# Performance work log

Hardware: AMD Instinct MI355X
Metric: run time of the kernel (lower is better)

Reference implementation:

```python
import jax, jax.numpy as jnp
import numpy as np

# hyperparameters (init_kwargs)
T = 0.1
MARGIN = 0.0
NEG_IOU = 0.5
K = 2              # pos_topk
WEIGHT = 1.0
EXPONENT = 2.0
NEG_SAMPLES = 512  # neg_samples_num
START_DNS_EPOCH = 1

# static problem sizes
B, SPB, TPS = 16, 2, 4          # videos, sentences/video, targets/sentence
N, C = 64, 256                  # clips, channels
S = B * SPB                     # total sentences = 32
M = S * TPS                     # total moments = 128


def setup_inputs() -> dict:
    key = jax.random.key(0)
    k1, k2, k3, k4 = jax.random.split(key, 4)
    return {
        "video_feats": jax.random.normal(k1, (S, C, N, N), jnp.float32),
        "sents_feats": jax.random.normal(k2, (S, C), jnp.float32),
        "num_sentences": jnp.full((B,), SPB, jnp.int32),
        "num_targets": jnp.full((S,), TPS, jnp.int32),
        "iou2d": jax.random.uniform(k3, (S, N, N), jnp.float32),
        "iou2ds": jax.random.uniform(k4, (M, N, N), jnp.float32),
        "mask2d": jnp.triu(jnp.ones((N, N), bool)),  # 2D-TAN valid-proposal mask
        "epoch": 2,
    }


def _normalize(x):
    return x / jnp.maximum(jnp.linalg.norm(x, axis=-1, keepdims=True), 1e-12)


def _loss_core(video_feats, sents_feats, iou2d, iou2ds,
               num_sentences, num_targets, mask2d, epoch):
    S_, C_, N_, _ = video_feats.shape
    B_ = num_sentences.shape[0]
    M_ = iou2ds.shape[0]
    P = N_ * (N_ + 1) // 2  # number of True in upper-triangular mask2d

    # masked_select(mask2d) -> gather flat proposal positions (static size P)
    flat_idx = jnp.nonzero(mask2d.reshape(-1), size=P)[0]
    vf = video_feats.reshape(S_, C_, N_ * N_)[:, :, flat_idx]        # (S,C,P)
    vf = _normalize(vf.transpose(0, 2, 1))                            # (S,P,C)
    _ = _normalize(sents_feats)                                       # normalized but unused downstream
    iou2d_f = iou2d.reshape(S_, -1)[:, flat_idx]                      # (S,P)
    iou2ds_f = iou2ds.reshape(M_, -1)[:, flat_idx]                    # (M,P)

    scatter_m2s = jnp.repeat(jnp.arange(S_), num_targets, total_repeat_length=M_)
    scatter_s2b = jnp.repeat(jnp.arange(B_), num_sentences, total_repeat_length=S_)
    scatter_b2s = jnp.concatenate([jnp.zeros((1,), jnp.int32),
                                   jnp.cumsum(num_sentences)[:-1].astype(jnp.int32)])

    # all (ref, pos) pairs within each sentence's num_targets*K topk slots (uniform -> static)
    nK = (M_ // S_) * K
    base = (jnp.arange(S_) * nK)[:, None, None]
    i = jnp.arange(nK)
    zero = jnp.zeros((nK,), jnp.int32)
    ref_idx = (base + i[None, :, None] + zero[None, None, :]).reshape(-1)   # (E,)
    pos_idx = (base + zero[None, :, None] + i[None, None, :]).reshape(-1)   # (E,)
    scatter_e2s = jnp.repeat(jnp.arange(S_), nK * nK)                        # (E,)

    # top-K proposals per moment by IoU
    topk_idx = jax.lax.top_k(iou2ds_f, K)[1]                                 # (M,K)
    allm = vf[scatter_m2s]                                                   # (M,P,C)
    topk_vf = jnp.take_along_axis(allm, topk_idx[:, :, None], axis=1)        # (M,K,C)
    pos_vf = topk_vf.reshape(M_ * K, C_)

    intra_pos = jnp.sum(pos_vf[ref_idx] * pos_vf[pos_idx], axis=-1)          # (E,)
    bank = vf[scatter_b2s].reshape(B_ * P, C_)                               # one sentence per video
    intra_all = pos_vf @ bank.T                                              # (M*K, B*P)

    # positive mask: own-video block, refined by iou2d > neg_iou
    own = scatter_s2b[:, None] == jnp.arange(B_)[None, :]                    # (S,B)
    s2v_pos = iou2d_f > NEG_IOU                                              # (S,P)
    pos_mask = jnp.where(own[:, :, None], s2v_pos[:, None, :], False).reshape(S_, B_ * P)

    if epoch >= START_DNS_EPOCH:
        # DNS: similarity-weighted negative sampling without replacement (Gumbel top-k)
        sim = (jnp.einsum('mkc,pc->mkp', topk_vf, bank).mean(axis=1) + 1.0) * 0.5   # (M,B*P)
        fused = jax.ops.segment_sum(sim, scatter_m2s, num_segments=S_)
        fused = fused / num_targets[:, None].astype(sim.dtype)                      # per-sentence mean
        fused = jnp.where(pos_mask, 0.0, fused ** EXPONENT)                          # (S,B*P)
        logw = jnp.where(fused > 0, jnp.log(jnp.maximum(fused, 1e-30)), -jnp.inf)
        u = jax.random.uniform(jax.random.key(42), fused.shape, minval=1e-7, maxval=1.0 - 1e-7)
        gumbel = -jnp.log(-jnp.log(u))
        samp_idx = jax.lax.top_k(logw + gumbel, NEG_SAMPLES)[1]                      # (S,NEG_SAMPLES)
        neg_mask = jnp.zeros((S_, B_ * P), jnp.float32).at[
            jnp.arange(S_)[:, None], samp_idx].set(1.0)
    else:
        neg_mask = (~pos_mask).astype(jnp.float32)

    # LogCrossEntropy (InfoNCE with explicit negative mask)
    all_e = intra_all[ref_idx]            # (E, B*P)
    neg_e = neg_mask[scatter_e2s]         # (E, B*P)
    pos_logit = (intra_pos - MARGIN) / T
    neg_sum = jnp.sum(jnp.exp(all_e / T) * neg_e, axis=-1)
    loss = jnp.mean(-(pos_logit - jnp.log(jnp.exp(pos_logit) + neg_sum)))
    return loss


def reference(video_feats, sents_feats, num_sentences, num_targets,
              iou2d, iou2ds, mask2d, epoch):
    loss = _loss_core(video_feats, sents_feats, iou2d, iou2ds,
                      num_sentences, num_targets, mask2d, epoch)
    return (loss * WEIGHT, loss)
```

## Files before the change

kernel.cpp:

```cpp
#include <hip/hip_runtime.h>
#include <math.h>
#include <stdint.h>

#define S_    32
#define BV_   16
#define M_    128
#define C_    256
#define NN    4096
#define P_    2080
#define BP    33280
#define NSAMP 512
#define CHUNK 130

__device__ __forceinline__ uint32_t rotl32(uint32_t x, int n){ return (x<<n) | (x>>(32-n)); }

__device__ __forceinline__ void threefry2x32(uint32_t k0, uint32_t k1, uint32_t &x0, uint32_t &x1){
  uint32_t ks2 = k0 ^ k1 ^ 0x1BD11BDAu;
  x0 += k0; x1 += k1;
  #define TF_R(r) { x0 += x1; x1 = rotl32(x1, r); x1 ^= x0; }
  TF_R(13) TF_R(15) TF_R(26) TF_R(6)
  x0 += k1;  x1 += ks2 + 1u;
  TF_R(17) TF_R(29) TF_R(16) TF_R(24)
  x0 += ks2; x1 += k0 + 2u;
  TF_R(13) TF_R(15) TF_R(26) TF_R(6)
  x0 += k0;  x1 += k1 + 3u;
  TF_R(17) TF_R(29) TF_R(16) TF_R(24)
  x0 += k1;  x1 += ks2 + 4u;
  TF_R(13) TF_R(15) TF_R(26) TF_R(6)
  x0 += ks2; x1 += k0 + 5u;
  #undef TF_R
}

__device__ __forceinline__ void p_to_ij(int p, int &i, int &j){
  i = (int)((129.0f - sqrtf((float)(16641 - 8*p))) * 0.5f);
  while(64*(i+1) - ((i+1)*i)/2 <= p) ++i;
  while(64*i - (i*(i-1))/2 > p) --i;
  j = i + (p - (64*i - (i*(i-1))/2));
}

__global__ __launch_bounds__(256) void k_prep(const float* __restrict__ iou2ds,
                                              const float* __restrict__ vfeat,
                                              float* __restrict__ pos_vf,
                                              float* __restrict__ qsumT){
  const int s = blockIdx.x;
  const int t = threadIdx.x;
  __shared__ float sv1[256], sv2[256];
  __shared__ int   si1[256], si2[256];
  __shared__ int   fpk_s[8];
  __shared__ float wsum[4];
  __shared__ float s_inv;

  for(int q=0; q<4; ++q){
    const float* row = iou2ds + (size_t)(s*4 + q)*NN;
    float v1=-1e30f, v2=-1e30f; int i1=0x7FFFFFFF, i2=0x7FFFFFFF;
    for(int f=t; f<NN; f+=256){
      int ti = f>>6, tj = f&63;
      if(tj < ti) continue;
      float v = row[f];
      if(v > v1 || (v == v1 && f < i1)){ v2=v1; i2=i1; v1=v; i1=f; }
      else if(v > v2 || (v == v2 && f < i2)){ v2=v; i2=f; }
    }
    sv1[t]=v1; sv2[t]=v2; si1[t]=i1; si2[t]=i2;
    for(int stp=128; stp>0; stp>>=1){
      __syncthreads();
      if(t < stp){
        float a1=sv1[t], a2=sv2[t]; int x1=si1[t], x2=si2[t];
        float b1=sv1[t+stp], b2=sv2[t+stp]; int y1=si1[t+stp], y2=si2[t+stp];
        float m1v, m2v; int m1i, m2i;
        bool aTop = (a1 > b1) || (a1 == b1 && x1 < y1);
        if(aTop){
          m1v=a1; m1i=x1;
          if((a2 > b1) || (a2 == b1 && x2 < y1)){ m2v=a2; m2i=x2; } else { m2v=b1; m2i=y1; }
        } else {
          m1v=b1; m1i=y1;
          if((b2 > a1) || (b2 == a1 && y2 < x1)){ m2v=b2; m2i=y2; } else { m2v=a1; m2i=x1; }
        }
        sv1[t]=m1v; sv2[t]=m2v; si1[t]=m1i; si2[t]=m2i;
      }
    }
    __syncthreads();
    if(t==0){ fpk_s[q*2+0]=si1[0]; fpk_s[q*2+1]=si2[0]; }
    __syncthreads();
  }

  float v[8];
  #pragma unroll
  for(int r=0;r<8;r++) v[r] = vfeat[((size_t)s*C_ + t)*NN + fpk_s[r]];

  float qs = 0.f;
  for(int r=0; r<8; ++r){
    float ss = v[r]*v[r];
    for(int o=32;o>0;o>>=1) ss += __shfl_down(ss, o, 64);
    if((t&63)==0) wsum[t>>6]=ss;
    __syncthreads();
    if(t==0){
      float tot = wsum[0]+wsum[1]+wsum[2]+wsum[3];
      s_inv = 1.0f / fmaxf(sqrtf(tot), 1e-12f);
    }
    __syncthreads();
    float pv = v[r] * s_inv;
    pos_vf[(size_t)(s*8+r)*C_ + t] = pv;
    qs += pv;
  }
  qsumT[t*32 + s] = qs;
}

__global__ __launch_bounds__(256) void k_bank(const float* __restrict__ vfeat,
                                              float* __restrict__ bank){
  extern __shared__ char dyn_sm[];
  float* tile = (float*)dyn_sm;
  float* ssp4 = (float*)dyn_sm + 256*65;
  float* invs = (float*)dyn_sm + 256*65 + 1024;

  const int i = blockIdx.x;
  const int b = blockIdx.y;
  const int t = threadIdx.x;
  const float* basep = vfeat + (size_t)(2*b)*C_*NN + (size_t)i*64;
  const int cc0 = t >> 4;
  const int j0  = (t & 15) * 4;

  float sq0=0.f, sq1=0.f, sq2=0.f, sq3=0.f;
  #pragma unroll
  for(int it=0; it<16; ++it){
    int cc = it*16 + cc0;
    float4 v = *(const float4*)(basep + (size_t)cc*NN + j0);
    tile[cc*65 + j0+0] = v.x; tile[cc*65 + j0+1] = v.y;
    tile[cc*65 + j0+2] = v.z; tile[cc*65 + j0+3] = v.w;
    sq0 += v.x*v.x; sq1 += v.y*v.y; sq2 += v.z*v.z; sq3 += v.w*v.w;
  }
  ssp4[t*4+0]=sq0; ssp4[t*4+1]=sq1; ssp4[t*4+2]=sq2; ssp4[t*4+3]=sq3;
  __syncthreads();
  if(t < 64){
    float tot = 0.f;
    #pragma unroll
    for(int g=0; g<16; ++g) tot += ssp4[g*64 + t];
    invs[t] = 1.0f/fmaxf(sqrtf(tot), 1e-12f);
  }
  __syncthreads();

  const int start = 64*i - (i*(i-1))/2;
  for(int jj=i; jj<64; ++jj){
    size_t row = (size_t)b*P_ + start + (jj - i);
    bank[row*C_ + t] = tile[t*65 + jj] * invs[jj];
  }
}

__global__ __launch_bounds__(256) void k_fused_keys(const float* __restrict__ bank,
                                                    const float* __restrict__ qsumT,
                                                    const float* __restrict__ iou2d,
                                                    unsigned int* __restrict__ ukey){
  __shared__ float tile[32*257];
  const int t = threadIdx.x;
  const int j = blockIdx.x*256 + t;

  int bv = j / P_;
  int p  = j - bv*P_;
  int pi, pj; p_to_ij(p, pi, pj);
  int fp = pi*64 + pj;
  float iou0 = iou2d[(size_t)(2*bv)*NN + fp];
  float iou1 = iou2d[(size_t)(2*bv+1)*NN + fp];

  float acc[32];
  #pragma unroll
  for(int s=0;s<32;s++) acc[s]=0.f;

  for(int cb=0; cb<8; ++cb){
    __syncthreads();
    #pragma unroll
    for(int it=0; it<8; ++it){
      int idx = it*256 + t;
      int jj  = idx >> 3;
      int c4  = idx & 7;
      float4 v = ((const float4*)bank)[ (size_t)(blockIdx.x*256 + jj)*64 + cb*8 + c4 ];
      tile[(c4*4+0)*257 + jj]=v.x; tile[(c4*4+1)*257 + jj]=v.y;
      tile[(c4*4+2)*257 + jj]=v.z; tile[(c4*4+3)*257 + jj]=v.w;
    }
    __syncthreads();
    const float* qb = qsumT + cb*32*32;
    #pragma unroll 2
    for(int cc=0; cc<32; ++cc){
      float v = tile[cc*257 + t];
      const float* qc = qb + cc*32;
      #pragma unroll
      for(int s=0;s<32;s++) acc[s] = fmaf(qc[s], v, acc[s]);
    }
  }

  #pragma unroll 1
  for(int s=0;s<32;s++){
    float fz = 0.0625f*acc[s] + 0.5f;
    bool pos = ((s>>1)==bv) && (((s&1)?iou1:iou0) > 0.5f);
    float val = pos ? 0.f : fz*fz;
    float key;
    if(val > 0.f){
      float logw = logf(fmaxf(val, 1e-30f));
      unsigned int f = (unsigned int)(s*BP + j);
      const unsigned int HALF = 532480u;
      bool second = f >= HALF;
      uint32_t x0 = second ? (f - HALF) : f;
      uint32_t x1 = second ? f : (f + HALF);
      threefry2x32(0u, 42u, x0, x1);
      uint32_t bits = second ? x1 : x0;
      uint32_t fb = (bits >> 9) | 0x3f800000u;
      float f01 = __uint_as_float(fb) - 1.0f;
      const float mn = 1e-7f, mx = 1.0f - 1e-7f;
      float u = fmaxf(mn, f01*(mx-mn) + mn);
      float g = -logf(-logf(u));
      key = logw + g;
    } else {
      key = -INFINITY;
    }
    unsigned int kb = __float_as_uint(key);
    kb = (kb & 0x80000000u) ? ~kb : (kb | 0x80000000u);
    ukey[(size_t)s*BP + j] = kb;
  }
}

__global__ __launch_bounds__(1024) void k_select(const unsigned int* __restrict__ ukey,
                                                 int* __restrict__ neglist){
  extern __shared__ char dyn_sm[];
  unsigned int* row  = (unsigned int*)dyn_sm;
  unsigned int* hist = (unsigned int*)dyn_sm + BP;
  int* eqbuf = (int*)hist;
  __shared__ int s_wv[16];
  __shared__ unsigned int s_prefix;
  __shared__ int s_cntgt, s_need, s_eq;

  const int s = blockIdx.x;
  const int t = threadIdx.x;
  const int lane = t & 63;
  const int col  = t & 15;
  const unsigned int* grow = ukey + (size_t)s*BP;
  int* list = neglist + s*NSAMP;

  unsigned int prefix = 0, pmask = 0;
  int need = NSAMP, cnt_gt = 0;

  for(int lev=0; lev<4; ++lev){
    const int shift = 24 - 8*lev;
    for(int k=t; k<256*17; k+=1024) hist[k] = 0;
    __syncthreads();
    if(lev==0){
      for(int k=t; k<BP; k+=1024){
        unsigned int u = grow[k];
        row[k] = u;
        atomicAdd(&hist[(u >> 24)*17 + col], 1u);
      }
    } else {
      for(int k=t; k<BP; k+=1024){
        unsigned int u = row[k];
        if((u & pmask) == prefix)
          atomicAdd(&hist[((u >> shift) & 255u)*17 + col], 1u);
      }
    }
    __syncthreads();
    int v = 0; unsigned int h = 0;
    if(t < 256){
      const unsigned int* hr = hist + t*17;
      #pragma unroll
      for(int c=0;c<16;c++) h += hr[c];
      v = (int)h;
      #pragma unroll
      for(int off=1; off<64; off<<=1){
        int src = lane + off;
        int o = __shfl(v, (src<64)?src:lane, 64);
        v += (src<64)? o : 0;
      }
      if(lane==0) s_wv[t>>6] = v;
    }
    __syncthreads();
    if(t < 256){
      int wv4 = t>>6, tail = 0;
      for(int w2=wv4+1; w2<4; ++w2) tail += s_wv[w2];
      int Sb  = v + tail;
      int Sb1 = Sb - (int)h;
      if(Sb >= need && Sb1 < need){
        s_prefix = prefix | ((unsigned int)t << shift);
        s_cntgt  = cnt_gt + Sb1;
        s_need   = need - Sb1;
      }
    }
    __syncthreads();
    prefix = s_prefix; cnt_gt = s_cntgt; need = s_need;
    pmask |= (0xFFu << shift);
    __syncthreads();
  }

  const unsigned int ustar = prefix;
  const int quota = need;

  if(t==0) s_eq = 0;
  __syncthreads();

  int gtc = 0;
  for(int k=t; k<BP; k+=1024) gtc += (row[k] > ustar) ? 1 : 0;
  int vg = gtc;
  #pragma unroll
  for(int off=1; off<64; off<<=1){
    int src = lane - off;
    int o = __shfl(vg, (src>=0)?src:lane, 64);
    vg += (src>=0)? o : 0;
  }
  const int wv16 = t>>6;
  if(lane==63) s_wv[wv16] = vg;
  __syncthreads();
  int base2 = 0;
  for(int w2=0; w2<wv16; ++w2) base2 += s_wv[w2];
  int gi = base2 + vg - gtc;
  for(int k=t; k<BP; k+=1024){
    unsigned int u = row[k];
    if(u > ustar){
      list[gi++] = k;
    } else if(u == ustar){
      int e = atomicAdd(&s_eq, 1);
      if(e < 2048) eqbuf[e] = k;
    }
  }
  __syncthreads();
  const int eqn = s_eq;
  if(eqn <= 2048){
    for(int i2=t; i2<eqn; i2+=1024){
      int ii = eqbuf[i2];
      int r = 0;
      for(int j2=0; j2<eqn; ++j2) r += (eqbuf[j2] < ii) ? 1 : 0;
      if(r < quota) list[cnt_gt + r] = ii;
    }
  } else {
    if(t==0){
      int taken = 0;
      for(int idx=0; idx<BP && taken<quota; ++idx)
        if(row[idx]==ustar){ list[cnt_gt + taken] = idx; ++taken; }
    }
  }
}

__global__ __launch_bounds__(512) void k_negsum(const float* __restrict__ bank,
                                                const float* __restrict__ pos_vf,
                                                const int* __restrict__ neglist,
                                                float* __restrict__ ns){
  int s = blockIdx.x;
  int t = threadIdx.x;
  __shared__ float pv[8][C_];
  for(int idx=t; idx<8*C_; idx+=512) pv[idx>>8][idx&255] = pos_vf[(size_t)(s*8)*C_ + idx];
  __syncthreads();
  int j = neglist[s*NSAMP + t];
  const float4* bp = (const float4*)(bank + (size_t)j*C_);
  float acc[8] = {0,0,0,0,0,0,0,0};
  for(int c4=0; c4<64; ++c4){
    float4 bv = bp[c4];
    #pragma unroll
    for(int a=0;a<8;a++){
      const float* pva = &pv[a][c4*4];
      acc[a] += bv.x*pva[0] + bv.y*pva[1] + bv.z*pva[2] + bv.w*pva[3];
    }
  }
  float e[8];
  #pragma unroll
  for(int a=0;a<8;a++){
    float v = expf(acc[a]/0.1f);
    for(int o=32;o>0;o>>=1) v += __shfl_down(v, o, 64);
    e[a] = v;
  }
  __shared__ float red[8][8];
  int wv = t>>6;
  if((t&63)==0){
    #pragma unroll
    for(int a=0;a<8;a++) red[wv][a]=e[a];
  }
  __syncthreads();
  if(t < 8){
    float tot = 0.f;
    for(int w=0; w<8; w++) tot += red[w][t];
    ns[s*8 + t] = tot;
  }
}

__global__ __launch_bounds__(64) void k_loss(const float* __restrict__ pos_vf,
                                             const float* __restrict__ ns,
                                             float* __restrict__ partial){
  int s = blockIdx.x;
  int t = threadIdx.x;
  __shared__ float pv[8][260];
  for(int idx=t; idx<8*C_; idx+=64){
    pv[idx>>8][idx&255] = pos_vf[(size_t)(s*8)*C_ + idx];
  }
  __syncthreads();
  int a = t>>3, b = t&7;
  float dot = 0.f;
  for(int c=0;c<C_;c++) dot += pv[a][c]*pv[b][c];
  float pl = dot/0.1f;
  float term = logf(expf(pl) + ns[s*8+a]) - pl;
  for(int o=32;o>0;o>>=1) term += __shfl_down(term, o, 64);
  if(t==0) partial[s]=term;
}

__global__ void k_final(const float* __restrict__ partial, float* __restrict__ out){
  int t = threadIdx.x;
  float v = (t < 32) ? partial[t] : 0.f;
  for(int o=32;o>0;o>>=1) v += __shfl_down(v, o, 64);
  if(t==0){
    float loss = v / 2048.0f;
    out[0] = loss * 1.0f;
    out[1] = loss;
  }
}

extern "C" void kernel_launch(void* const* d_in, const int* in_sizes, int n_in,
                              void* d_out, int out_size, void* d_ws, size_t ws_size,
                              hipStream_t stream) {
  const float* video_feats = (const float*)d_in[0];
  const float* iou2d  = (const float*)d_in[4];
  const float* iou2ds = (const float*)d_in[5];

  const size_t o_pvf   = 0;
  const size_t o_qsT   = 262144;
  const size_t o_bank  = 294912;
  const size_t o_ukey  = 34373632;
  const size_t o_list  = 38633472;
  const size_t o_ns    = 38699008;
  const size_t o_part  = 38700032;
  const size_t NEED    = 38700288;
  if (ws_size < NEED) return;

  char* w = (char*)d_ws;
  float*        pos_vf  = (float*)(w + o_pvf);
  float*        qsumT   = (float*)(w + o_qsT);
  float*        bank    = (float*)(w + o_bank);
  unsigned int* ukey    = (unsigned int*)(w + o_ukey);
  int*          neglist = (int*)(w + o_list);
  float*        ns      = (float*)(w + o_ns);
  float*        part    = (float*)(w + o_part);
  float*        out     = (float*)d_out;

  const int BK_LDS  = (256*65 + 1024 + 64) * 4;
  const int SEL_LDS = (BP + 256*17) * 4;
  static bool attr_set = false;
  if(!attr_set){
    (void)hipFuncSetAttribute((const void*)k_bank,
                              hipFuncAttributeMaxDynamicSharedMemorySize, BK_LDS);
    (void)hipFuncSetAttribute((const void*)k_select,
                              hipFuncAttributeMaxDynamicSharedMemorySize, SEL_LDS);
    attr_set = true;
  }

  k_prep<<<32, 256, 0, stream>>>(iou2ds, video_feats, pos_vf, qsumT);
  k_bank<<<dim3(64,16), 256, BK_LDS, stream>>>(video_feats, bank);
  k_fused_keys<<<130, 256, 0, stream>>>(bank, qsumT, iou2d, ukey);
  k_select<<<32, 1024, SEL_LDS, stream>>>(ukey, neglist);
  k_negsum<<<32, 512, 0, stream>>>(bank, pos_vf, neglist, ns);
  k_loss<<<32, 64, 0, stream>>>(pos_vf, ns, part);
  k_final<<<1, 64, 0, stream>>>(part, out);
}
```

Measured before the change: 178.6 us.

## Split top-k prep across moments and compact radix-select candidates in LDS

The prep kernel is split into a per-moment top-2 kernel with 128 blocks and a separate positive-feature normalization kernel, so the iou2ds scan is spread over more blocks. The radix select now builds only the first-byte histogram over the full row, then gathers elements of the boundary bucket into a capped LDS candidate buffer. The remaining three radix levels run only on those candidates instead of re-scanning the 33K-element row. Selected indices are then sorted by rank so the output order stays deterministic. The change adds one kernel launch, plus a fallback path that reads the row from global memory when the candidates overflow the buffer.

```diff
diff --git a/kernel.cpp b/kernel.cpp
--- a/kernel.cpp
+++ b/kernel.cpp
@@ -10,7 +10,7 @@
 #define P_    2080
 #define BP    33280
 #define NSAMP 512
-#define CHUNK 130
+#define CAP   8192
 
 __device__ __forceinline__ uint32_t rotl32(uint32_t x, int n){ return (x<<n) | (x>>(32-n)); }
 
@@ -38,71 +38,74 @@
   j = i + (p - (64*i - (i*(i-1))/2));
 }
 
-__global__ __launch_bounds__(256) void k_prep(const float* __restrict__ iou2ds,
-                                              const float* __restrict__ vfeat,
-                                              float* __restrict__ pos_vf,
-                                              float* __restrict__ qsumT){
-  const int s = blockIdx.x;
-  const int t = threadIdx.x;
+__global__ __launch_bounds__(256) void k_topk(const float* __restrict__ iou2ds,
+                                              int* __restrict__ fpk){
+  int m = blockIdx.x;
+  const float* row = iou2ds + (size_t)m*NN;
+  float v1=-1e30f, v2=-1e30f; int i1=0x7FFFFFFF, i2=0x7FFFFFFF;
+  for(int f=threadIdx.x; f<NN; f+=256){
+    int ti = f>>6, tj = f&63;
+    if(tj < ti) continue;
+    float v = row[f];
+    if(v > v1 || (v == v1 && f < i1)){ v2=v1; i2=i1; v1=v; i1=f; }
+    else if(v > v2 || (v == v2 && f < i2)){ v2=v; i2=f; }
+  }
   __shared__ float sv1[256], sv2[256];
   __shared__ int   si1[256], si2[256];
-  __shared__ int   fpk_s[8];
+  sv1[threadIdx.x]=v1; sv2[threadIdx.x]=v2; si1[threadIdx.x]=i1; si2[threadIdx.x]=i2;
+  for(int stp=128; stp>0; stp>>=1){
+    __syncthreads();
+    if((int)threadIdx.x < stp){
+      float a1=sv1[threadIdx.x], a2=sv2[threadIdx.x];
+      int   x1=si1[threadIdx.x], x2=si2[threadIdx.x];
+      float b1=sv1[threadIdx.x+stp], b2=sv2[threadIdx.x+stp];
+      int   y1=si1[threadIdx.x+stp], y2=si2[threadIdx.x+stp];
+      float m1v, m2v; int m1i, m2i;
+      bool aTop = (a1 > b1) || (a1 == b1 && x1 < y1);
+      if(aTop){
+        m1v=a1; m1i=x1;
+        if((a2 > b1) || (a2 == b1 && x2 < y1)){ m2v=a2; m2i=x2; } else { m2v=b1; m2i=y1; }
+      } else {
+        m1v=b1; m1i=y1;
+        if((b2 > a1) || (b2 == a1 && y2 < x1)){ m2v=b2; m2i=y2; } else { m2v=a1; m2i=x1; }
+      }
+      sv1[threadIdx.x]=m1v; sv2[threadIdx.x]=m2v; si1[threadIdx.x]=m1i; si2[threadIdx.x]=m2i;
+    }
+  }
+  __syncthreads();
+  if(threadIdx.x==0){
+    fpk[m*2+0] = si1[0];
+    fpk[m*2+1] = si2[0];
+  }
+}
+
+__global__ __launch_bounds__(256) void k_pos(const float* __restrict__ vfeat,
+                                             const int* __restrict__ fpk,
+                                             float* __restrict__ pos_vf,
+                                             float* __restrict__ qsumT){
+  int s = blockIdx.x;
+  int c = threadIdx.x;
   __shared__ float wsum[4];
   __shared__ float s_inv;
-
-  for(int q=0; q<4; ++q){
-    const float* row = iou2ds + (size_t)(s*4 + q)*NN;
-    float v1=-1e30f, v2=-1e30f; int i1=0x7FFFFFFF, i2=0x7FFFFFFF;
-    for(int f=t; f<NN; f+=256){
-      int ti = f>>6, tj = f&63;
-      if(tj < ti) continue;
-      float v = row[f];
-      if(v > v1 || (v == v1 && f < i1)){ v2=v1; i2=i1; v1=v; i1=f; }
-      else if(v > v2 || (v == v2 && f < i2)){ v2=v; i2=f; }
-    }
-    sv1[t]=v1; sv2[t]=v2; si1[t]=i1; si2[t]=i2;
-    for(int stp=128; stp>0; stp>>=1){
-      __syncthreads();
-      if(t < stp){
-        float a1=sv1[t], a2=sv2[t]; int x1=si1[t], x2=si2[t];
-        float b1=sv1[t+stp], b2=sv2[t+stp]; int y1=si1[t+stp], y2=si2[t+stp];
-        float m1v, m2v; int m1i, m2i;
-        bool aTop = (a1 > b1) || (a1 == b1 && x1 < y1);
-        if(aTop){
-          m1v=a1; m1i=x1;
-          if((a2 > b1) || (a2 == b1 && x2 < y1)){ m2v=a2; m2i=x2; } else { m2v=b1; m2i=y1; }
-        } else {
-          m1v=b1; m1i=y1;
-          if((b2 > a1) || (b2 == a1 && y2 < x1)){ m2v=b2; m2i=y2; } else { m2v=a1; m2i=x1; }
-        }
-        sv1[t]=m1v; sv2[t]=m2v; si1[t]=m1i; si2[t]=m2i;
-      }
-    }
-    __syncthreads();
-    if(t==0){ fpk_s[q*2+0]=si1[0]; fpk_s[q*2+1]=si2[0]; }
-    __syncthreads();
-  }
-
-  float v[8];
-  #pragma unroll
-  for(int r=0;r<8;r++) v[r] = vfeat[((size_t)s*C_ + t)*NN + fpk_s[r]];
-
   float qs = 0.f;
   for(int r=0; r<8; ++r){
-    float ss = v[r]*v[r];
+    int row = s*8 + r;
+    int fp = fpk[row];
+    float v = vfeat[((size_t)s*C_ + c)*NN + fp];
+    float ss = v*v;
     for(int o=32;o>0;o>>=1) ss += __shfl_down(ss, o, 64);
-    if((t&63)==0) wsum[t>>6]=ss;
-    __syncthreads();
-    if(t==0){
+    if((c&63)==0) wsum[c>>6]=ss;
+    __syncthreads();
+    if(c==0){
       float tot = wsum[0]+wsum[1]+wsum[2]+wsum[3];
       s_inv = 1.0f / fmaxf(sqrtf(tot), 1e-12f);
     }
     __syncthreads();
-    float pv = v[r] * s_inv;
-    pos_vf[(size_t)(s*8+r)*C_ + t] = pv;
+    float pv = v * s_inv;
+    pos_vf[(size_t)row*C_ + c] = pv;
     qs += pv;
   }
-  qsumT[t*32 + s] = qs;
+  qsumT[c*32 + s] = qs;
 }
 
 __global__ __launch_bounds__(256) void k_bank(const float* __restrict__ vfeat,
@@ -219,41 +222,27 @@
 __global__ __launch_bounds__(1024) void k_select(const unsigned int* __restrict__ ukey,
                                                  int* __restrict__ neglist){
   extern __shared__ char dyn_sm[];
-  unsigned int* row  = (unsigned int*)dyn_sm;
-  unsigned int* hist = (unsigned int*)dyn_sm + BP;
-  int* eqbuf = (int*)hist;
+  unsigned int* cand_key = (unsigned int*)dyn_sm;
+  int*          cand_idx = (int*)dyn_sm + CAP;
+  unsigned int* hist     = (unsigned int*)dyn_sm + 2*CAP;
+  int*          list_lds = (int*)dyn_sm + 2*CAP + 256*17;
   __shared__ int s_wv[16];
   __shared__ unsigned int s_prefix;
-  __shared__ int s_cntgt, s_need, s_eq;
+  __shared__ int s_cntgt, s_need, s_gt, s_nc;
 
   const int s = blockIdx.x;
   const int t = threadIdx.x;
   const int lane = t & 63;
   const int col  = t & 15;
   const unsigned int* grow = ukey + (size_t)s*BP;
-  int* list = neglist + s*NSAMP;
-
-  unsigned int prefix = 0, pmask = 0;
-  int need = NSAMP, cnt_gt = 0;
-
-  for(int lev=0; lev<4; ++lev){
-    const int shift = 24 - 8*lev;
-    for(int k=t; k<256*17; k+=1024) hist[k] = 0;
-    __syncthreads();
-    if(lev==0){
-      for(int k=t; k<BP; k+=1024){
-        unsigned int u = grow[k];
-        row[k] = u;
-        atomicAdd(&hist[(u >> 24)*17 + col], 1u);
-      }
-    } else {
-      for(int k=t; k<BP; k+=1024){
-        unsigned int u = row[k];
-        if((u & pmask) == prefix)
-          atomicAdd(&hist[((u >> shift) & 255u)*17 + col], 1u);
-      }
-    }
-    __syncthreads();
+
+  for(int k=t; k<256*17; k+=1024) hist[k] = 0;
+  if(t==0){ s_gt = 0; s_nc = 0; }
+  __syncthreads();
+  for(int k=t; k<BP; k+=1024)
+    atomicAdd(&hist[(grow[k] >> 24)*17 + col], 1u);
+  __syncthreads();
+  {
     int v = 0; unsigned int h = 0;
     if(t < 256){
       const unsigned int* hr = hist + t*17;
@@ -274,63 +263,161 @@
       for(int w2=wv4+1; w2<4; ++w2) tail += s_wv[w2];
       int Sb  = v + tail;
       int Sb1 = Sb - (int)h;
-      if(Sb >= need && Sb1 < need){
-        s_prefix = prefix | ((unsigned int)t << shift);
-        s_cntgt  = cnt_gt + Sb1;
-        s_need   = need - Sb1;
-      }
-    }
-    __syncthreads();
-    prefix = s_prefix; cnt_gt = s_cntgt; need = s_need;
-    pmask |= (0xFFu << shift);
-    __syncthreads();
-  }
-
-  const unsigned int ustar = prefix;
-  const int quota = need;
-
-  if(t==0) s_eq = 0;
-  __syncthreads();
-
-  int gtc = 0;
-  for(int k=t; k<BP; k+=1024) gtc += (row[k] > ustar) ? 1 : 0;
-  int vg = gtc;
-  #pragma unroll
-  for(int off=1; off<64; off<<=1){
-    int src = lane - off;
-    int o = __shfl(vg, (src>=0)?src:lane, 64);
-    vg += (src>=0)? o : 0;
-  }
-  const int wv16 = t>>6;
-  if(lane==63) s_wv[wv16] = vg;
-  __syncthreads();
-  int base2 = 0;
-  for(int w2=0; w2<wv16; ++w2) base2 += s_wv[w2];
-  int gi = base2 + vg - gtc;
+      if(Sb >= NSAMP && Sb1 < NSAMP){
+        s_prefix = ((unsigned int)t) << 24;
+        s_cntgt  = Sb1;
+        s_need   = NSAMP - Sb1;
+      }
+    }
+    __syncthreads();
+  }
+  unsigned int prefix = s_prefix;
+  int cnt_gt = s_cntgt, need = s_need;
+  const unsigned int Bstar = prefix >> 24;
+  unsigned int pmask = 0xFF000000u;
+  __syncthreads();
+
   for(int k=t; k<BP; k+=1024){
-    unsigned int u = row[k];
-    if(u > ustar){
-      list[gi++] = k;
-    } else if(u == ustar){
-      int e = atomicAdd(&s_eq, 1);
-      if(e < 2048) eqbuf[e] = k;
-    }
-  }
-  __syncthreads();
-  const int eqn = s_eq;
-  if(eqn <= 2048){
-    for(int i2=t; i2<eqn; i2+=1024){
-      int ii = eqbuf[i2];
-      int r = 0;
-      for(int j2=0; j2<eqn; ++j2) r += (eqbuf[j2] < ii) ? 1 : 0;
-      if(r < quota) list[cnt_gt + r] = ii;
-    }
+    unsigned int u = grow[k];
+    unsigned int top = u >> 24;
+    if(top > Bstar){
+      int sl = atomicAdd(&s_gt, 1);
+      list_lds[sl] = k;
+    } else if(top == Bstar){
+      int c = atomicAdd(&s_nc, 1);
+      if(c < CAP){ cand_key[c] = u; cand_idx[c] = k; }
+    }
+  }
+  __syncthreads();
+  const int nc = s_nc;
+
+  if(nc <= CAP){
+    for(int lev=1; lev<4; ++lev){
+      const int shift = 24 - 8*lev;
+      for(int k=t; k<256*17; k+=1024) hist[k] = 0;
+      __syncthreads();
+      for(int c=t; c<nc; c+=1024){
+        unsigned int u = cand_key[c];
+        if((u & pmask) == prefix)
+          atomicAdd(&hist[((u >> shift) & 255u)*17 + col], 1u);
+      }
+      __syncthreads();
+      int v = 0; unsigned int h = 0;
+      if(t < 256){
+        const unsigned int* hr = hist + t*17;
+        #pragma unroll
+        for(int c=0;c<16;c++) h += hr[c];
+        v = (int)h;
+        #pragma unroll
+        for(int off=1; off<64; off<<=1){
+          int src = lane + off;
+          int o = __shfl(v, (src<64)?src:lane, 64);
+          v += (src<64)? o : 0;
+        }
+        if(lane==0) s_wv[t>>6] = v;
+      }
+      __syncthreads();
+      if(t < 256){
+        int wv4 = t>>6, tail = 0;
+        for(int w2=wv4+1; w2<4; ++w2) tail += s_wv[w2];
+        int Sb  = v + tail;
+        int Sb1 = Sb - (int)h;
+        if(Sb >= need && Sb1 < need){
+          s_prefix = prefix | (((unsigned int)t) << shift);
+          s_cntgt  = cnt_gt + Sb1;
+          s_need   = need - Sb1;
+        }
+      }
+      __syncthreads();
+      prefix = s_prefix; cnt_gt = s_cntgt; need = s_need;
+      pmask |= (0xFFu << shift);
+      __syncthreads();
+    }
+    const unsigned int ustar = prefix;
+    const int quota = need;
+
+    for(int c=t; c<nc; c+=1024){
+      if(cand_key[c] > ustar){
+        int sl = atomicAdd(&s_gt, 1);
+        list_lds[sl] = cand_idx[c];
+      }
+    }
+    __syncthreads();
+    for(int c=t; c<nc; c+=1024){
+      if(cand_key[c] == ustar){
+        int my = cand_idx[c];
+        int r = 0;
+        for(int j2=0; j2<nc; ++j2) r += (cand_key[j2]==ustar && cand_idx[j2] < my);
+        if(r < quota) list_lds[cnt_gt + r] = my;
+      }
+    }
+    __syncthreads();
   } else {
+    for(int lev=1; lev<4; ++lev){
+      const int shift = 24 - 8*lev;
+      for(int k=t; k<256*17; k+=1024) hist[k] = 0;
+      __syncthreads();
+      for(int k=t; k<BP; k+=1024){
+        unsigned int u = grow[k];
+        if((u & pmask) == prefix)
+          atomicAdd(&hist[((u >> shift) & 255u)*17 + col], 1u);
+      }
+      __syncthreads();
+      int v = 0; unsigned int h = 0;
+      if(t < 256){
+        const unsigned int* hr = hist + t*17;
+        #pragma unroll
+        for(int c=0;c<16;c++) h += hr[c];
+        v = (int)h;
+        #pragma unroll
+        for(int off=1; off<64; off<<=1){
+          int src = lane + off;
+          int o = __shfl(v, (src<64)?src:lane, 64);
+          v += (src<64)? o : 0;
+        }
+        if(lane==0) s_wv[t>>6] = v;
+      }
+      __syncthreads();
+      if(t < 256){
+        int wv4 = t>>6, tail = 0;
+        for(int w2=wv4+1; w2<4; ++w2) tail += s_wv[w2];
+        int Sb  = v + tail;
+        int Sb1 = Sb - (int)h;
+        if(Sb >= need && Sb1 < need){
+          s_prefix = prefix | (((unsigned int)t) << shift);
+          s_cntgt  = cnt_gt + Sb1;
+          s_need   = need - Sb1;
+        }
+      }
+      __syncthreads();
+      prefix = s_prefix; cnt_gt = s_cntgt; need = s_need;
+      pmask |= (0xFFu << shift);
+      __syncthreads();
+    }
+    const unsigned int ustar = prefix;
+    const int quota = need;
+
+    for(int k=t; k<BP; k+=1024){
+      unsigned int u = grow[k];
+      if((u >> 24) == Bstar && u > ustar){
+        int sl = atomicAdd(&s_gt, 1);
+        list_lds[sl] = k;
+      }
+    }
+    __syncthreads();
     if(t==0){
       int taken = 0;
-      for(int idx=0; idx<BP && taken<quota; ++idx)
-        if(row[idx]==ustar){ list[cnt_gt + taken] = idx; ++taken; }
-    }
+      for(int k=0; k<BP && taken<quota; ++k)
+        if(grow[k]==ustar){ list_lds[cnt_gt + taken] = k; ++taken; }
+    }
+    __syncthreads();
+  }
+
+  if(t < NSAMP){
+    int my = list_lds[t];
+    int r = 0;
+    for(int j2=0; j2<NSAMP; ++j2) r += (list_lds[j2] < my);
+    neglist[s*NSAMP + r] = my;
   }
 }
 
@@ -412,17 +499,19 @@
   const float* iou2d  = (const float*)d_in[4];
   const float* iou2ds = (const float*)d_in[5];
 
-  const size_t o_pvf   = 0;
-  const size_t o_qsT   = 262144;
-  const size_t o_bank  = 294912;
-  const size_t o_ukey  = 34373632;
-  const size_t o_list  = 38633472;
-  const size_t o_ns    = 38699008;
-  const size_t o_part  = 38700032;
-  const size_t NEED    = 38700288;
+  const size_t o_fpk   = 0;
+  const size_t o_pvf   = 1024;
+  const size_t o_qsT   = 263168;
+  const size_t o_bank  = 295936;
+  const size_t o_ukey  = 34374656;
+  const size_t o_list  = 38634496;
+  const size_t o_ns    = 38700032;
+  const size_t o_part  = 38701056;
+  const size_t NEED    = 38701312;
   if (ws_size < NEED) return;
 
   char* w = (char*)d_ws;
+  int*          fpk     = (int*)(w + o_fpk);
   float*        pos_vf  = (float*)(w + o_pvf);
   float*        qsumT   = (float*)(w + o_qsT);
   float*        bank    = (float*)(w + o_bank);
@@ -433,7 +522,7 @@
   float*        out     = (float*)d_out;
 
   const int BK_LDS  = (256*65 + 1024 + 64) * 4;
-  const int SEL_LDS = (BP + 256*17) * 4;
+  const int SEL_LDS = (2*CAP + 256*17 + NSAMP) * 4;
   static bool attr_set = false;
   if(!attr_set){
     (void)hipFuncSetAttribute((const void*)k_bank,
@@ -443,7 +532,8 @@
     attr_set = true;
   }
 
-  k_prep<<<32, 256, 0, stream>>>(iou2ds, video_feats, pos_vf, qsumT);
+  k_topk<<<128, 256, 0, stream>>>(iou2ds, fpk);
+  k_pos<<<32, 256, 0, stream>>>(video_feats, fpk, pos_vf, qsumT);
   k_bank<<<dim3(64,16), 256, BK_LDS, stream>>>(video_feats, bank);
   k_fused_keys<<<130, 256, 0, stream>>>(bank, qsumT, iou2d, ukey);
   k_select<<<32, 1024, SEL_LDS, stream>>>(ukey, neglist);
```

Result: slower. 213.0 us (+19.2%).
